# Optimization experiments

Hardware: AMD Instinct MI355X
Metric: run time of the kernel (lower is better)

## Reference

```python
import jax, jax.numpy as jnp
import numpy as np

EPS_RMS = 1e-6
EPS_L2 = 1e-12  # torch F.normalize default eps


def _l2_normalize(x):
    n = jnp.sqrt(jnp.sum(x * x, axis=-1, keepdims=True))
    return x / jnp.maximum(n, EPS_L2)


def _dwconv(x, w, b):
    # depthwise Conv1d: x [B,L,D], w [D,1,K], b [D]; padding=K//2 (same length for odd K)
    K = w.shape[-1]
    y = jax.lax.conv_general_dilated(
        jnp.swapaxes(x, 1, 2), w, window_strides=(1,),
        padding=[(K // 2, K // 2)], feature_group_count=w.shape[0],
        dimension_numbers=('NCH', 'OIH', 'NCH'))
    return jnp.swapaxes(y + b[None, :, None], 1, 2)


def setup_inputs() -> dict:
    key = jax.random.key(0)
    ks = jax.random.split(key, 12)
    B, L, D, K = 8, 2048, 128, 3
    inp = {
        'x': jax.random.normal(ks[0], (B, L, D), dtype=jnp.float32),
        'state': jnp.zeros((B, D, D), dtype=jnp.float32),
        'W_in': jax.random.normal(ks[1], (4 * D, D), dtype=jnp.float32) * 0.02,
        'W_gate': jax.random.normal(ks[2], (2 * D, D), dtype=jnp.float32) * 0.02,
        'W_out': jax.random.normal(ks[3], (D, D), dtype=jnp.float32) * 0.02,
        'W_res': jax.random.normal(ks[4], (D, D), dtype=jnp.float32) * 0.02,
        'qconv_w': jax.random.normal(ks[5], (D, 1, K), dtype=jnp.float32) * 0.5,
        'qconv_b': jnp.zeros((D,), dtype=jnp.float32),
        'kconv_w': jax.random.normal(ks[6], (D, 1, K), dtype=jnp.float32) * 0.5,
        'kconv_b': jnp.zeros((D,), dtype=jnp.float32),
        'rms_w': jnp.ones((D,), dtype=jnp.float32),
    }
    return inp


def reference(x, state, W_in, W_gate, W_out, W_res,
              qconv_w, qconv_b, kconv_w, kconv_b, rms_w):
    B, L, D = x.shape
    residual = x @ W_res.T
    qkv = x @ W_in.T  # [B,L,4D]
    q, k, v, gate = jnp.split(qkv, 4, axis=-1)
    q = _l2_normalize(jax.nn.sigmoid(_dwconv(q, qconv_w, qconv_b)))
    k = _l2_normalize(jax.nn.sigmoid(_dwconv(k, kconv_w, kconv_b)))
    g = jax.nn.sigmoid(gate @ W_gate.T)  # [B,L,2D]
    alpha, beta = jnp.split(g, 2, axis=-1)

    # Delta-rule recurrence over time. State S [B,D,D] indexed S[b, v_dim, k_dim]:
    # S <- alpha_j * (S_ij - (S k)_i * beta_j k_j) + beta_j * v_i k_j ; out = silu(q @ S)
    def step(S, inp):
        q_t, k_t, v_t, a_t, b_t = inp  # each [B,D]
        Sk = jnp.einsum('bij,bj->bi', S, k_t)          # S @ k
        bk = b_t * k_t                                  # beta*k, column scaling
        S = a_t[:, None, :] * (S - Sk[:, :, None] * bk[:, None, :]) \
            + v_t[:, :, None] * bk[:, None, :]
        out_t = jax.nn.silu(jnp.einsum('bi,bij->bj', q_t, S))
        return S, out_t

    xs = tuple(jnp.swapaxes(a, 0, 1) for a in (q, k, v, alpha, beta))  # [L,B,D]
    S_fin, outs = jax.lax.scan(step, state, xs)
    out = jnp.swapaxes(outs, 0, 1) @ W_out.T  # [B,L,D]
    # dropout (p=0.125) is identity in eval mode
    out = out * jax.lax.rsqrt(jnp.mean(out * out, axis=-1, keepdims=True) + EPS_RMS) * rms_w
    out = out + residual
    return out, S_fin
```

## Files before the change

kernel.cpp:

```cpp
#include <hip/hip_runtime.h>
#include <hip/hip_bf16.h>
#include <math.h>

#define BB 8
#define LL 2048
#define LH 1024
#define DD 128

template <int CTRL>
__device__ __forceinline__ float dpp_add(float x) {
    int xi = __float_as_int(x);
    int yi = __builtin_amdgcn_update_dpp(xi, xi, CTRL, 0xF, 0xF, false);
    return x + __int_as_float(yi);
}
__device__ __forceinline__ float allreduce16(float p) {
    p = dpp_add<0xB1>(p);
    p = dpp_add<0x4E>(p);
    p = dpp_add<0x141>(p);
    p = dpp_add<0x140>(p);
    return p;
}
__device__ __forceinline__ float rlane(float p, int l) {
    return __int_as_float(__builtin_amdgcn_readlane(__float_as_int(p), l));
}

__global__ __launch_bounds__(256) void gemm_kernel(
    const float* __restrict__ X, long ldx, long sB, long sH,
    const float* __restrict__ W,
    float* __restrict__ C, int ldc,
    int applySig)
{
    __shared__ float Xs[32 * 132];
    __shared__ float Ws[64 * 132];
    const int tid = threadIdx.x;
    const int m0 = blockIdx.x * 32;
    const int o0 = blockIdx.y * 64;
    {
        int row = tid >> 3, cg = tid & 7;
        int m = m0 + row;
        int b = m >> 11, t = m & 2047, h = t >> 10, tl = t & 1023;
        const float* src = X + (size_t)b * sB + (size_t)h * sH
                             + (size_t)tl * ldx + cg * 16;
        float* dst = Xs + row * 132 + cg * 16;
#pragma unroll
        for (int u = 0; u < 4; ++u)
            *(float4*)(dst + 4 * u) = *(const float4*)(src + 4 * u);
    }
    {
        int o = tid >> 2, cg = tid & 3;
        const float* src = W + (size_t)(o0 + o) * 128 + cg * 32;
        float* dst = Ws + o * 132 + cg * 32;
#pragma unroll
        for (int u = 0; u < 8; ++u)
            *(float4*)(dst + 4 * u) = *(const float4*)(src + 4 * u);
    }
    __syncthreads();
    const int tx = tid & 31, ty = tid >> 5;
    float acc[4][2] = {};
    const float* xb = Xs + (ty * 4) * 132;
    const float* wb = Ws + (tx * 2) * 132;
    for (int k0 = 0; k0 < 128; k0 += 4) {
        float4 xr[4], wr[2];
#pragma unroll
        for (int r = 0; r < 4; ++r) xr[r] = *(const float4*)(xb + r * 132 + k0);
#pragma unroll
        for (int cc = 0; cc < 2; ++cc) wr[cc] = *(const float4*)(wb + cc * 132 + k0);
#pragma unroll
        for (int r = 0; r < 4; ++r)
#pragma unroll
            for (int cc = 0; cc < 2; ++cc) {
                acc[r][cc] += xr[r].x * wr[cc].x + xr[r].y * wr[cc].y
                            + xr[r].z * wr[cc].z + xr[r].w * wr[cc].w;
            }
    }
#pragma unroll
    for (int r = 0; r < 4; ++r)
#pragma unroll
        for (int cc = 0; cc < 2; ++cc) {
            float v = acc[r][cc];
            if (applySig) v = 1.0f / (1.0f + __expf(-v));
            C[(size_t)(m0 + ty * 4 + r) * ldc + o0 + tx * 2 + cc] = v;
        }
}

__global__ __launch_bounds__(256) void convnorm_kernel(
    const float* __restrict__ qkv,
    const float* __restrict__ qw, const float* __restrict__ qb,
    const float* __restrict__ kw, const float* __restrict__ kb,
    const float* __restrict__ ab,
    float* __restrict__ pack)
{
    const int tid = threadIdx.x;
    const int lane = tid & 63;
    const int wid = tid >> 6;
    const int m = blockIdx.x * 4 + wid;
    const int l = m & (LL - 1);
    const int b = m >> 11;
    const int d0 = lane * 2;
    float yq0 = qb[d0], yq1 = qb[d0 + 1];
    float yk0 = kb[d0], yk1 = kb[d0 + 1];
#pragma unroll
    for (int tau = 0; tau < 3; ++tau) {
        int lp = l + tau - 1;
        if (lp >= 0 && lp < LL) {
            const float* base = qkv + (size_t)(m + tau - 1) * 512;
            yq0 += base[d0]       * qw[d0 * 3 + tau];
            yq1 += base[d0 + 1]   * qw[(d0 + 1) * 3 + tau];
            yk0 += base[128 + d0]     * kw[d0 * 3 + tau];
            yk1 += base[128 + d0 + 1] * kw[(d0 + 1) * 3 + tau];
        }
    }
    yq0 = 1.0f / (1.0f + __expf(-yq0));
    yq1 = 1.0f / (1.0f + __expf(-yq1));
    yk0 = 1.0f / (1.0f + __expf(-yk0));
    yk1 = 1.0f / (1.0f + __expf(-yk1));
    float sq = yq0 * yq0 + yq1 * yq1;
    float sk = yk0 * yk0 + yk1 * yk1;
#pragma unroll
    for (int msk = 1; msk <= 32; msk <<= 1) {
        sq += __shfl_xor(sq, msk);
        sk += __shfl_xor(sk, msk);
    }
    float rq = 1.0f / fmaxf(sqrtf(sq), 1e-12f);
    float rk = 1.0f / fmaxf(sqrtf(sk), 1e-12f);
    float k0n = yk0 * rk, k1n = yk1 * rk;
    float a0 = ab[(size_t)m * 256 + d0];
    float a1 = ab[(size_t)m * 256 + d0 + 1];
    float b0 = ab[(size_t)m * 256 + 128 + d0];
    float b1 = ab[(size_t)m * 256 + 128 + d0 + 1];
    float v0 = qkv[(size_t)m * 512 + 256 + d0];
    float v1 = qkv[(size_t)m * 512 + 256 + d0 + 1];
    float* P = pack + ((size_t)b * 512 + (l >> 2)) * 2560 + (l & 3);
    P[d0 * 4]              = k0n;      P[(d0 + 1) * 4]        = k1n;
    P[512 + d0 * 4]        = b0 * k0n; P[512 + (d0 + 1) * 4]  = b1 * k1n;
    P[1024 + d0 * 4]       = a0;       P[1024 + (d0 + 1) * 4] = a1;
    P[1536 + d0 * 4]       = yq0 * rq; P[1536 + (d0 + 1) * 4] = yq1 * rq;
    P[2048 + d0 * 4]       = v0;       P[2048 + (d0 + 1) * 4] = v1;
}

__global__ __launch_bounds__(64, 1) void recur2_kernel(
    const float* __restrict__ pack, const float* __restrict__ sin,
    __hip_bfloat16* __restrict__ pout, float* __restrict__ sout, int blk0)
{
    const int lane = threadIdx.x;
    const int b = blockIdx.x >> 6;
    const int g = blockIdx.x & 63;
    const int rbase = g * 2;
    const int iA = lane >> 5;
    const int c  = lane & 31;
    const int colA = c * 4;
    const int j0 = lane * 2;

    float SA[4];
    {
        const float* sp = sin + ((size_t)b * DD + rbase + iA) * DD + colA;
        float4 t4 = *(const float4*)sp;
        SA[0] = t4.x; SA[1] = t4.y; SA[2] = t4.z; SA[3] = t4.w;
    }
    float SB[2][2];
#pragma unroll
    for (int r = 0; r < 2; ++r) {
        const float* sp = sin + ((size_t)b * DD + rbase + r) * DD + j0;
        float2 t2 = *(const float2*)(sp);
        SB[r][0] = t2.x; SB[r][1] = t2.y;
    }

    const float* P = pack + ((size_t)b * 512 + blk0) * 2560;
    __hip_bfloat16* po = pout + ((size_t)g * (BB * LH) + (size_t)b * LH) * DD + j0;

    float4 ka4[2][4], ma4[2][4], aa4[2][4];
    float4 qv4[2][2], vv4[2][2], aB4[2][2], mB4[2][2];

#define PREB(BF)                                                             \
    do {                                                                     \
        _Pragma("unroll")                                                    \
        for (int u = 0; u < 4; ++u) {                                        \
            ka4[BF][u] = *(const float4*)(P + (colA + u) * 4);               \
            ma4[BF][u] = *(const float4*)(P + 512 + (colA + u) * 4);         \
            aa4[BF][u] = *(const float4*)(P + 1024 + (colA + u) * 4);        \
        }                                                                    \
        qv4[BF][0] = *(const float4*)(P + 1536 + rbase * 4);                 \
        qv4[BF][1] = *(const float4*)(P + 1536 + rbase * 4 + 4);             \
        vv4[BF][0] = *(const float4*)(P + 2048 + rbase * 4);                 \
        vv4[BF][1] = *(const float4*)(P + 2048 + rbase * 4 + 4);             \
        aB4[BF][0] = *(const float4*)(P + 1024 + j0 * 4);                    \
        aB4[BF][1] = *(const float4*)(P + 1024 + j0 * 4 + 4);                \
        mB4[BF][0] = *(const float4*)(P + 512 + j0 * 4);                     \
        mB4[BF][1] = *(const float4*)(P + 512 + j0 * 4 + 4);                 \
        P += 2560;                                                           \
        __builtin_amdgcn_sched_barrier(0);         \
    } while (0)

#define STEPQ(BF, CMP)                                                       \
    do {                                                                     \
        float e0 = SA[0] * ka4[BF][0].CMP;                                   \
        float e1 = SA[1] * ka4[BF][1].CMP;                                   \
        e0 = fmaf(SA[2], ka4[BF][2].CMP, e0);                                \
        e1 = fmaf(SA[3], ka4[BF][3].CMP, e1);                                \
        float p = e0 + e1;                                                   \
        p = allreduce16(p);                                                  \
        float sk0 = rlane(p, 0)  + rlane(p, 16);                             \
        float sk1 = rlane(p, 32) + rlane(p, 48);                             \
        float pown = iA ? sk1 : sk0;                                         \
        float vA   = iA ? vv4[BF][1].CMP : vv4[BF][0].CMP;                   \
        _Pragma("unroll")                                                    \
        for (int u = 0; u < 4; ++u) {                                        \
            float au = aa4[BF][u].CMP;                                       \
            float w = fmaf(-au, pown, vA);                                   \
            SA[u] = fmaf(ma4[BF][u].CMP, w, au * SA[u]);                     \
        }                                                                    \
        float aB0 = aB4[BF][0].CMP, aB1 = aB4[BF][1].CMP;                    \
        float mB0 = mB4[BF][0].CMP, mB1 = mB4[BF][1].CMP;                    \
        float po0 = 0.0f, po1 = 0.0f;                                        \
        _Pragma("unroll")                                                    \
        for (int r = 0; r < 2; ++r) {                                        \
            float skr = r ? sk1 : sk0;                                       \
            float vvr = r ? vv4[BF][1].CMP : vv4[BF][0].CMP;                 \
            float qvr = r ? qv4[BF][1].CMP : qv4[BF][0].CMP;                 \
            float w0 = fmaf(-aB0, skr, vvr);                                 \
            SB[r][0] = fmaf(mB0, w0, aB0 * SB[r][0]);                        \
            po0 = fmaf(qvr, SB[r][0], po0);                                  \
            float w1 = fmaf(-aB1, skr, vvr);                                 \
            SB[r][1] = fmaf(mB1, w1, aB1 * SB[r][1]);                        \
            po1 = fmaf(qvr, SB[r][1], po1);                                  \
        }                                                                    \
        __hip_bfloat162 h2;                                                  \
        h2.x = __float2bfloat16(po0);                                        \
        h2.y = __float2bfloat16(po1);                                        \
        *(__hip_bfloat162*)po = h2;                                          \
        po += DD;                                                            \
    } while (0)

#define STEP4(BF) \
    do { STEPQ(BF, x); STEPQ(BF, y); STEPQ(BF, z); STEPQ(BF, w); } while (0)

    PREB(0);
    PREB(1);
    for (int tb = 0; tb < LH / 4; tb += 2) {
        STEP4(0);
        PREB(0);
        STEP4(1);
        PREB(1);
    }
#undef PREB
#undef STEPQ
#undef STEP4

    {
        float* sp = sout + ((size_t)b * DD + rbase + iA) * DD + colA;
        float4 o4 = {SA[0], SA[1], SA[2], SA[3]};
        *(float4*)sp = o4;
    }
}

__global__ __launch_bounds__(256) void combine_silu_kernel(
    const ushort* __restrict__ pout, float* __restrict__ ocbase, int h)
{
    const size_t NHALF = (size_t)BB * LH * DD;
    size_t idx = ((size_t)blockIdx.x * 256 + threadIdx.x) * 4;
    float s0 = 0, s1 = 0, s2 = 0, s3 = 0;
#pragma unroll 8
    for (int gi = 0; gi < 64; ++gi) {
        uint2 u = *(const uint2*)(pout + gi * NHALF + idx);
        s0 += __uint_as_float((u.x & 0xffffu) << 16);
        s1 += __uint_as_float(u.x & 0xffff0000u);
        s2 += __uint_as_float((u.y & 0xffffu) << 16);
        s3 += __uint_as_float(u.y & 0xffff0000u);
    }
    float4 r;
    r.x = s0 / (1.0f + __expf(-s0));
    r.y = s1 / (1.0f + __expf(-s1));
    r.z = s2 / (1.0f + __expf(-s2));
    r.w = s3 / (1.0f + __expf(-s3));
    size_t b = idx >> 17;
    size_t rem = idx & ((size_t)LH * DD - 1);
    float* dst = ocbase + b * (2048ull * 640) + (size_t)h * (1024ull * 640) + rem;
    *(float4*)dst = r;
}

__global__ __launch_bounds__(256) void rms_res_kernel(
    const float* __restrict__ y, const float* __restrict__ res,
    const float* __restrict__ rmsw, float* __restrict__ out)
{
    const int tid = threadIdx.x;
    const int lane = tid & 63;
    const int wid = tid >> 6;
    const int m = blockIdx.x * 4 + wid;
    const int d0 = lane * 2;
    size_t o = (size_t)m * DD + d0;
    float2 yv = *(const float2*)(y + o);
    float ss = yv.x * yv.x + yv.y * yv.y;
#pragma unroll
    for (int msk = 1; msk <= 32; msk <<= 1) ss += __shfl_xor(ss, msk);
    float r = rsqrtf(ss * (1.0f / 128.0f) + 1e-6f);
    float2 rv = *(const float2*)(res + o);
    out[o]     = yv.x * r * rmsw[d0]     + rv.x;
    out[o + 1] = yv.y * r * rmsw[d0 + 1] + rv.y;
}

extern "C" void kernel_launch(void* const* d_in, const int* in_sizes, int n_in,
                              void* d_out, int out_size, void* d_ws, size_t ws_size,
                              hipStream_t stream)
{
    const float* x      = (const float*)d_in[0];
    const float* state  = (const float*)d_in[1];
    const float* W_in   = (const float*)d_in[2];
    const float* W_gate = (const float*)d_in[3];
    const float* W_out  = (const float*)d_in[4];
    const float* W_res  = (const float*)d_in[5];
    const float* qcw    = (const float*)d_in[6];
    const float* qcb    = (const float*)d_in[7];
    const float* kcw    = (const float*)d_in[8];
    const float* kcb    = (const float*)d_in[9];
    const float* rmsw   = (const float*)d_in[10];
    float* out  = (float*)d_out;
    float* sfin = out + (size_t)BB * LL * DD;

    const size_t M = (size_t)BB * LL;
    char* base = (char*)d_ws;
    const size_t PACK_BYTES = M * 640 * 4;
    float* pack = (float*)base;
    char*  poreg = base + PACK_BYTES;
    float* qkv = (float*)poreg;
    float* abv = (float*)(poreg + M * 512 * 4);
    __hip_bfloat16* po = (__hip_bfloat16*)poreg;
    float* res = (float*)poreg;
    float* yb  = (float*)(poreg + M * DD * 4);

    const long ld128 = 128, ld512 = 512;
    dim3 blk(256);
    gemm_kernel<<<dim3(M / 32, 8), blk, 0, stream>>>(
        x, ld128, 2048 * ld128, 1024 * ld128, W_in, qkv, 512, 0);
    gemm_kernel<<<dim3(M / 32, 4), blk, 0, stream>>>(
        qkv + 384, ld512, 2048 * ld512, 1024 * ld512, W_gate, abv, 256, 1);
    convnorm_kernel<<<dim3(M / 4), blk, 0, stream>>>(qkv, qcw, qcb, kcw, kcb, abv, pack);
    recur2_kernel<<<dim3(BB * 64), dim3(64), 0, stream>>>(pack, state, po, sfin, 0);
    combine_silu_kernel<<<dim3((BB * LH * DD) / 1024), blk, 0, stream>>>(
        (const ushort*)po, pack, 0);
    recur2_kernel<<<dim3(BB * 64), dim3(64), 0, stream>>>(pack, sfin, po, sfin, 256);
    combine_silu_kernel<<<dim3((BB * LH * DD) / 1024), blk, 0, stream>>>(
        (const ushort*)po, pack, 1);
    gemm_kernel<<<dim3(M / 32, 2), blk, 0, stream>>>(
        x, ld128, 2048 * ld128, 1024 * ld128, W_res, res, 128, 0);
    gemm_kernel<<<dim3(M / 32, 2), blk, 0, stream>>>(
        pack, ld128, 2048 * 640, 1024 * 640, W_out, yb, 128, 0);
    rms_res_kernel<<<dim3(M / 4), blk, 0, stream>>>(yb, res, rmsw, out);
}
```

Measured before the change: 614.5 us.

## Split recurrence into one-row-per-wave blocks over four time chunks

The recurrence kernel now gives each 64-lane wave a single state row (1024 blocks instead of 512), which removes the duplicated SB bookkeeping and cuts per-step work and register pressure. The sequence is processed in four 512-step chunks instead of two 1024-step halves, so the bf16 partial-output buffer still fits in the workspace. Combine now sums 128 partials instead of 64, and the GEMM address mapping is updated for quarter-sequence chunks. The trade-off is more kernel launches, more serial chunk boundaries and more partial-output traffic through combine.

```diff
diff --git a/kernel.cpp b/kernel.cpp
--- a/kernel.cpp
+++ b/kernel.cpp
@@ -4,7 +4,7 @@
 
 #define BB 8
 #define LL 2048
-#define LH 1024
+#define LQ 512
 #define DD 128
 
 template <int CTRL>
@@ -25,7 +25,7 @@
 }
 
 __global__ __launch_bounds__(256) void gemm_kernel(
-    const float* __restrict__ X, long ldx, long sB, long sH,
+    const float* __restrict__ X, long ldx, long sB, long sQ,
     const float* __restrict__ W,
     float* __restrict__ C, int ldc,
     int applySig)
@@ -38,8 +38,8 @@
     {
         int row = tid >> 3, cg = tid & 7;
         int m = m0 + row;
-        int b = m >> 11, t = m & 2047, h = t >> 10, tl = t & 1023;
-        const float* src = X + (size_t)b * sB + (size_t)h * sH
+        int b = m >> 11, t = m & 2047, qq = t >> 9, tl = t & 511;
+        const float* src = X + (size_t)b * sB + (size_t)qq * sQ
                              + (size_t)tl * ldx + cg * 16;
         float* dst = Xs + row * 132 + cg * 16;
 #pragma unroll
@@ -138,95 +138,58 @@
     P[2048 + d0 * 4]       = v0;       P[2048 + (d0 + 1) * 4] = v1;
 }
 
-__global__ __launch_bounds__(64, 1) void recur2_kernel(
+__global__ __launch_bounds__(64, 1) void recur1_kernel(
     const float* __restrict__ pack, const float* __restrict__ sin,
     __hip_bfloat16* __restrict__ pout, float* __restrict__ sout, int blk0)
 {
     const int lane = threadIdx.x;
-    const int b = blockIdx.x >> 6;
-    const int g = blockIdx.x & 63;
-    const int rbase = g * 2;
-    const int iA = lane >> 5;
-    const int c  = lane & 31;
-    const int colA = c * 4;
+    const int b = blockIdx.x >> 7;
+    const int g = blockIdx.x & 127;
     const int j0 = lane * 2;
 
-    float SA[4];
+    float SA[2];
     {
-        const float* sp = sin + ((size_t)b * DD + rbase + iA) * DD + colA;
-        float4 t4 = *(const float4*)sp;
-        SA[0] = t4.x; SA[1] = t4.y; SA[2] = t4.z; SA[3] = t4.w;
-    }
-    float SB[2][2];
-#pragma unroll
-    for (int r = 0; r < 2; ++r) {
-        const float* sp = sin + ((size_t)b * DD + rbase + r) * DD + j0;
-        float2 t2 = *(const float2*)(sp);
-        SB[r][0] = t2.x; SB[r][1] = t2.y;
+        const float* sp = sin + ((size_t)b * DD + g) * DD + j0;
+        float2 t2 = *(const float2*)sp;
+        SA[0] = t2.x; SA[1] = t2.y;
     }
 
     const float* P = pack + ((size_t)b * 512 + blk0) * 2560;
-    __hip_bfloat16* po = pout + ((size_t)g * (BB * LH) + (size_t)b * LH) * DD + j0;
-
-    float4 ka4[2][4], ma4[2][4], aa4[2][4];
-    float4 qv4[2][2], vv4[2][2], aB4[2][2], mB4[2][2];
+    __hip_bfloat16* po = pout + ((size_t)g * (BB * LQ) + (size_t)b * LQ) * DD + j0;
+
+    float4 ka4[2][2], ma4[2][2], aa4[2][2];
+    float4 qv4[2], vv4[2];
 
 #define PREB(BF)                                                             \
     do {                                                                     \
-        _Pragma("unroll")                                                    \
-        for (int u = 0; u < 4; ++u) {                                        \
-            ka4[BF][u] = *(const float4*)(P + (colA + u) * 4);               \
-            ma4[BF][u] = *(const float4*)(P + 512 + (colA + u) * 4);         \
-            aa4[BF][u] = *(const float4*)(P + 1024 + (colA + u) * 4);        \
-        }                                                                    \
-        qv4[BF][0] = *(const float4*)(P + 1536 + rbase * 4);                 \
-        qv4[BF][1] = *(const float4*)(P + 1536 + rbase * 4 + 4);             \
-        vv4[BF][0] = *(const float4*)(P + 2048 + rbase * 4);                 \
-        vv4[BF][1] = *(const float4*)(P + 2048 + rbase * 4 + 4);             \
-        aB4[BF][0] = *(const float4*)(P + 1024 + j0 * 4);                    \
-        aB4[BF][1] = *(const float4*)(P + 1024 + j0 * 4 + 4);                \
-        mB4[BF][0] = *(const float4*)(P + 512 + j0 * 4);                     \
-        mB4[BF][1] = *(const float4*)(P + 512 + j0 * 4 + 4);                 \
+        ka4[BF][0] = *(const float4*)(P + j0 * 4);                           \
+        ka4[BF][1] = *(const float4*)(P + j0 * 4 + 4);                       \
+        ma4[BF][0] = *(const float4*)(P + 512 + j0 * 4);                     \
+        ma4[BF][1] = *(const float4*)(P + 512 + j0 * 4 + 4);                 \
+        aa4[BF][0] = *(const float4*)(P + 1024 + j0 * 4);                    \
+        aa4[BF][1] = *(const float4*)(P + 1024 + j0 * 4 + 4);                \
+        qv4[BF]    = *(const float4*)(P + 1536 + g * 4);                     \
+        vv4[BF]    = *(const float4*)(P + 2048 + g * 4);                     \
         P += 2560;                                                           \
         __builtin_amdgcn_sched_barrier(0);         \
     } while (0)
 
 #define STEPQ(BF, CMP)                                                       \
     do {                                                                     \
-        float e0 = SA[0] * ka4[BF][0].CMP;                                   \
-        float e1 = SA[1] * ka4[BF][1].CMP;                                   \
-        e0 = fmaf(SA[2], ka4[BF][2].CMP, e0);                                \
-        e1 = fmaf(SA[3], ka4[BF][3].CMP, e1);                                \
-        float p = e0 + e1;                                                   \
-        p = allreduce16(p);                                                  \
-        float sk0 = rlane(p, 0)  + rlane(p, 16);                             \
-        float sk1 = rlane(p, 32) + rlane(p, 48);                             \
-        float pown = iA ? sk1 : sk0;                                         \
-        float vA   = iA ? vv4[BF][1].CMP : vv4[BF][0].CMP;                   \
-        _Pragma("unroll")                                                    \
-        for (int u = 0; u < 4; ++u) {                                        \
-            float au = aa4[BF][u].CMP;                                       \
-            float w = fmaf(-au, pown, vA);                                   \
-            SA[u] = fmaf(ma4[BF][u].CMP, w, au * SA[u]);                     \
-        }                                                                    \
-        float aB0 = aB4[BF][0].CMP, aB1 = aB4[BF][1].CMP;                    \
-        float mB0 = mB4[BF][0].CMP, mB1 = mB4[BF][1].CMP;                    \
-        float po0 = 0.0f, po1 = 0.0f;                                        \
-        _Pragma("unroll")                                                    \
-        for (int r = 0; r < 2; ++r) {                                        \
-            float skr = r ? sk1 : sk0;                                       \
-            float vvr = r ? vv4[BF][1].CMP : vv4[BF][0].CMP;                 \
-            float qvr = r ? qv4[BF][1].CMP : qv4[BF][0].CMP;                 \
-            float w0 = fmaf(-aB0, skr, vvr);                                 \
-            SB[r][0] = fmaf(mB0, w0, aB0 * SB[r][0]);                        \
-            po0 = fmaf(qvr, SB[r][0], po0);                                  \
-            float w1 = fmaf(-aB1, skr, vvr);                                 \
-            SB[r][1] = fmaf(mB1, w1, aB1 * SB[r][1]);                        \
-            po1 = fmaf(qvr, SB[r][1], po1);                                  \
-        }                                                                    \
+        float e = SA[0] * ka4[BF][0].CMP;                                    \
+        e = fmaf(SA[1], ka4[BF][1].CMP, e);                                  \
+        float p = allreduce16(e);                                            \
+        float sk = (rlane(p, 0) + rlane(p, 16))                              \
+                 + (rlane(p, 32) + rlane(p, 48));                            \
+        float vg = vv4[BF].CMP, qg = qv4[BF].CMP;                            \
+        float a0 = aa4[BF][0].CMP, a1 = aa4[BF][1].CMP;                      \
+        float w0 = fmaf(-a0, sk, vg);                                        \
+        SA[0] = fmaf(ma4[BF][0].CMP, w0, a0 * SA[0]);                        \
+        float w1 = fmaf(-a1, sk, vg);                                        \
+        SA[1] = fmaf(ma4[BF][1].CMP, w1, a1 * SA[1]);                        \
         __hip_bfloat162 h2;                                                  \
-        h2.x = __float2bfloat16(po0);                                        \
-        h2.y = __float2bfloat16(po1);                                        \
+        h2.x = __float2bfloat16(qg * SA[0]);                                 \
+        h2.y = __float2bfloat16(qg * SA[1]);                                 \
         *(__hip_bfloat162*)po = h2;                                          \
         po += DD;                                                            \
     } while (0)
@@ -236,7 +199,7 @@
 
     PREB(0);
     PREB(1);
-    for (int tb = 0; tb < LH / 4; tb += 2) {
+    for (int tb = 0; tb < LQ / 4; tb += 2) {
         STEP4(0);
         PREB(0);
         STEP4(1);
@@ -247,21 +210,21 @@
 #undef STEP4
 
     {
-        float* sp = sout + ((size_t)b * DD + rbase + iA) * DD + colA;
-        float4 o4 = {SA[0], SA[1], SA[2], SA[3]};
-        *(float4*)sp = o4;
+        float* sp = sout + ((size_t)b * DD + g) * DD + j0;
+        float2 o2 = {SA[0], SA[1]};
+        *(float2*)sp = o2;
     }
 }
 
 __global__ __launch_bounds__(256) void combine_silu_kernel(
-    const ushort* __restrict__ pout, float* __restrict__ ocbase, int h)
-{
-    const size_t NHALF = (size_t)BB * LH * DD;
+    const ushort* __restrict__ pout, float* __restrict__ ocbase, int q)
+{
+    const size_t NQ = (size_t)BB * LQ * DD;
     size_t idx = ((size_t)blockIdx.x * 256 + threadIdx.x) * 4;
     float s0 = 0, s1 = 0, s2 = 0, s3 = 0;
 #pragma unroll 8
-    for (int gi = 0; gi < 64; ++gi) {
-        uint2 u = *(const uint2*)(pout + gi * NHALF + idx);
+    for (int gi = 0; gi < 128; ++gi) {
+        uint2 u = *(const uint2*)(pout + gi * NQ + idx);
         s0 += __uint_as_float((u.x & 0xffffu) << 16);
         s1 += __uint_as_float(u.x & 0xffff0000u);
         s2 += __uint_as_float((u.y & 0xffffu) << 16);
@@ -272,9 +235,9 @@
     r.y = s1 / (1.0f + __expf(-s1));
     r.z = s2 / (1.0f + __expf(-s2));
     r.w = s3 / (1.0f + __expf(-s3));
-    size_t b = idx >> 17;
-    size_t rem = idx & ((size_t)LH * DD - 1);
-    float* dst = ocbase + b * (2048ull * 640) + (size_t)h * (1024ull * 640) + rem;
+    size_t b = idx >> 16;
+    size_t rem = idx & ((size_t)LQ * DD - 1);
+    float* dst = ocbase + b * (512ull * 2560) + (size_t)q * (128ull * 2560) + rem;
     *(float4*)dst = r;
 }
 
@@ -327,22 +290,22 @@
     float* res = (float*)poreg;
     float* yb  = (float*)(poreg + M * DD * 4);
 
-    const long ld128 = 128, ld512 = 512;
     dim3 blk(256);
     gemm_kernel<<<dim3(M / 32, 8), blk, 0, stream>>>(
-        x, ld128, 2048 * ld128, 1024 * ld128, W_in, qkv, 512, 0);
+        x, 128, 2048L * 128, 512L * 128, W_in, qkv, 512, 0);
     gemm_kernel<<<dim3(M / 32, 4), blk, 0, stream>>>(
-        qkv + 384, ld512, 2048 * ld512, 1024 * ld512, W_gate, abv, 256, 1);
+        qkv + 384, 512, 2048L * 512, 512L * 512, W_gate, abv, 256, 1);
     convnorm_kernel<<<dim3(M / 4), blk, 0, stream>>>(qkv, qcw, qcb, kcw, kcb, abv, pack);
-    recur2_kernel<<<dim3(BB * 64), dim3(64), 0, stream>>>(pack, state, po, sfin, 0);
-    combine_silu_kernel<<<dim3((BB * LH * DD) / 1024), blk, 0, stream>>>(
-        (const ushort*)po, pack, 0);
-    recur2_kernel<<<dim3(BB * 64), dim3(64), 0, stream>>>(pack, sfin, po, sfin, 256);
-    combine_silu_kernel<<<dim3((BB * LH * DD) / 1024), blk, 0, stream>>>(
-        (const ushort*)po, pack, 1);
+    for (int q = 0; q < 4; ++q) {
+        const float* sin = (q == 0) ? state : sfin;
+        recur1_kernel<<<dim3(BB * 128), dim3(64), 0, stream>>>(
+            pack, sin, po, sfin, q * 128);
+        combine_silu_kernel<<<dim3(512), blk, 0, stream>>>(
+            (const ushort*)po, pack, q);
+    }
     gemm_kernel<<<dim3(M / 32, 2), blk, 0, stream>>>(
-        x, ld128, 2048 * ld128, 1024 * ld128, W_res, res, 128, 0);
+        x, 128, 2048L * 128, 512L * 128, W_res, res, 128, 0);
     gemm_kernel<<<dim3(M / 32, 2), blk, 0, stream>>>(
-        pack, ld128, 2048 * 640, 1024 * 640, W_out, yb, 128, 0);
+        pack, 128, 512L * 2560, 128L * 2560, W_out, yb, 128, 0);
     rms_res_kernel<<<dim3(M / 4), blk, 0, stream>>>(yb, res, rmsw, out);
 }
```

Result: faster. 562.7 us (-8.4%).
